# Performance work log

Hardware: AMD Instinct MI355X
Metric: run time of the kernel (lower is better)

## Reference

```python
import jax, jax.numpy as jnp
import numpy as np

N_EMBD = 256
HIDDEN = 20  # hardcoded in the module
B, L = 4096, 64


def setup_inputs() -> dict:
    key = jax.random.key(0)
    ks = jax.random.split(key, 12)
    s = 0.02
    return {
        "key": jax.random.normal(ks[0], (B, L, N_EMBD), dtype=jnp.float32),
        "value": jax.random.normal(ks[1], (B, L, N_EMBD), dtype=jnp.float32),
        "query": jax.random.normal(ks[2], (B, L, N_EMBD), dtype=jnp.float32),
        "Wk": jax.random.normal(ks[3], (N_EMBD, HIDDEN), dtype=jnp.float32) * s,
        "bk": jnp.zeros((HIDDEN,), dtype=jnp.float32),
        "Wq": jax.random.normal(ks[4], (N_EMBD, HIDDEN), dtype=jnp.float32) * s,
        "bq": jnp.zeros((HIDDEN,), dtype=jnp.float32),
        "Wv": jax.random.normal(ks[5], (N_EMBD, HIDDEN), dtype=jnp.float32) * s,
        "bv": jnp.zeros((HIDDEN,), dtype=jnp.float32),
        "Wp": jax.random.normal(ks[6], (HIDDEN, N_EMBD), dtype=jnp.float32) * s,
        "bp": jnp.zeros((N_EMBD,), dtype=jnp.float32),
    }


def reference(key, value, query, Wk, bk, Wq, bq, Wv, bv, Wp, bp):
    # projections: [B, L, D] -> [B, L, 20]
    ks = key @ Wk + bk
    qs = query @ Wq + bq
    vs = value @ Wv + bv

    # torch code normalizes by GLOBAL Frobenius norm iff both sums are nonzero
    cond = (jnp.sum(qs) != 0) & (jnp.sum(ks) != 0)
    qs = jnp.where(cond, qs / jnp.linalg.norm(qs), qs)
    ks = jnp.where(cond, ks / jnp.linalg.norm(ks), ks)

    N = qs.shape[0]  # B acts as the 'node' / reduction axis
    # kvs: reduce over dim0 ('l' in torch einsum) -> [L, m, d]
    kvs = jnp.einsum('nlm,nld->lmd', ks, vs)
    attention_num = jnp.einsum('nlm,lmd->nld', qs, kvs)  # [B, L, 20]
    attention_num = attention_num + jnp.sum(vs, axis=0)  # + vs_sum [L, 20]

    ks_sum = jnp.sum(ks, axis=0)  # [L, 20]
    attention_normalizer = jnp.einsum('nlm,lm->nl', qs, ks_sum)[..., None]  # [B, L, 1]
    attention_normalizer = attention_normalizer + jnp.asarray(N, dtype=qs.dtype)

    attn_output = attention_num / attention_normalizer  # [B, L, 20]
    return attn_output @ Wp + bp  # [B, L, D]
```

## Files before the change

kernel.cpp:

```cpp
#include <hip/hip_runtime.h>


namespace {
constexpr int D    = 256;
constexpr int H    = 20;
constexpr int LDIM = 64;
constexpr int BDIM = 4096;
constexpr int BL   = BDIM * LDIM;
constexpr int TPB  = 256;
constexpr int KC   = 64;
constexpr int TS   = 257;

constexpr int OFF_KVS  = 0;
constexpr int OFF_KSUM = OFF_KVS + LDIM * H * H;
constexpr int OFF_VSUM = OFF_KSUM + LDIM * H;
constexpr int OFF_SCAL = OFF_VSUM + LDIM * H;
constexpr int ACC_FLOATS = OFF_SCAL + 4;
constexpr int OFF_QS   = 28416;
}

__device__ __forceinline__ void project_one(
    const float* __restrict__ in, const float* __restrict__ W,
    const float* __restrict__ bias, float* __restrict__ out,
    float* tile, int base, int tid,
    float* sum_dst, float* ss_dst)
{
    float acc[H];
#pragma unroll
    for (int m = 0; m < H; ++m) acc[m] = 0.f;

    const float4* __restrict__ in4 = reinterpret_cast<const float4*>(in);

    for (int c = 0; c < 4; ++c) {
#pragma unroll
        for (int i = 0; i < 16; ++i) {
            int f = tid + i * TPB;
            int token = f >> 4;
            int kq    = f & 15;
            float4 v = in4[(size_t)(base + token) * (D / 4) + c * 16 + kq];
            int kk = kq * 4;
            tile[(kk + 0) * TS + token] = v.x;
            tile[(kk + 1) * TS + token] = v.y;
            tile[(kk + 2) * TS + token] = v.z;
            tile[(kk + 3) * TS + token] = v.w;
        }
        __syncthreads();

        const float* __restrict__ Wc = W + c * KC * H;
#pragma unroll 2
        for (int k = 0; k < KC; ++k) {
            float x = tile[k * TS + tid];
#pragma unroll
            for (int m = 0; m < H; ++m)
                acc[m] = fmaf(x, Wc[k * H + m], acc[m]);
        }
        __syncthreads();
    }

    float v[H];
    float s1 = 0.f, s2 = 0.f;
#pragma unroll
    for (int m = 0; m < H; ++m) {
        v[m] = acc[m] + bias[m];
        s1 += v[m];
        s2 = fmaf(v[m], v[m], s2);
    }
    float4* o4 = reinterpret_cast<float4*>(out + (size_t)(base + tid) * H);
    o4[0] = make_float4(v[0],  v[1],  v[2],  v[3]);
    o4[1] = make_float4(v[4],  v[5],  v[6],  v[7]);
    o4[2] = make_float4(v[8],  v[9],  v[10], v[11]);
    o4[3] = make_float4(v[12], v[13], v[14], v[15]);
    o4[4] = make_float4(v[16], v[17], v[18], v[19]);

    if (sum_dst) {
#pragma unroll
        for (int off = 32; off > 0; off >>= 1) {
            s1 += __shfl_down(s1, off);
            s2 += __shfl_down(s2, off);
        }
        if ((tid & 63) == 0) {
            atomicAdd(sum_dst, s1);
            atomicAdd(ss_dst, s2);
        }
    }
}

__global__ __launch_bounds__(TPB) void proj_kernel(
    const float* __restrict__ key, const float* __restrict__ value,
    const float* __restrict__ query,
    const float* __restrict__ Wk, const float* __restrict__ bk,
    const float* __restrict__ Wq, const float* __restrict__ bq,
    const float* __restrict__ Wv, const float* __restrict__ bv,
    float* __restrict__ qs, float* __restrict__ ks, float* __restrict__ vs,
    float* __restrict__ scalars)
{
    __shared__ float tile[KC * TS];
    const int tid  = threadIdx.x;
    const int base = blockIdx.x * TPB;

    project_one(key,   Wk, bk, ks, tile, base, tid, scalars + 1, scalars + 3);
    project_one(value, Wv, bv, vs, tile, base, tid, nullptr,     nullptr);
    project_one(query, Wq, bq, qs, tile, base, tid, scalars + 0, scalars + 2);
}

__global__ __launch_bounds__(TPB) void reduce_kernel(
    const float* __restrict__ ks, const float* __restrict__ vs,
    float* __restrict__ kvs, float* __restrict__ ks_sum, float* __restrict__ vs_sum)
{
    __shared__ float lks[64 * H];
    __shared__ float lvs[64 * H];
    const int tid   = threadIdx.x;
    const int l     = blockIdx.x & 63;
    const int split = blockIdx.x >> 6;
    const int n0    = split * 64;

    const float4* __restrict__ ks4 = reinterpret_cast<const float4*>(ks);
    const float4* __restrict__ vs4 = reinterpret_cast<const float4*>(vs);
    float4* lks4 = reinterpret_cast<float4*>(lks);
    float4* lvs4 = reinterpret_cast<float4*>(lvs);
    for (int id = tid; id < 64 * (H / 4); id += TPB) {
        int n = id / (H / 4), q = id % (H / 4);
        size_t g = ((size_t)(n0 + n) * LDIM + l) * (H / 4) + q;
        lks4[id] = ks4[g];
        lvs4[id] = vs4[g];
    }
    __syncthreads();

    const int s0 = tid, s1 = tid + 256;
    const int m0 = s0 / H, d0 = s0 % H;
    const int m1 = s1 / H, d1 = s1 % H;
    const bool has1 = (s1 < H * H);
    float a0 = 0.f, a1 = 0.f;
    for (int n = 0; n < 64; ++n) {
        const float* pk = lks + n * H;
        const float* pv = lvs + n * H;
        a0 = fmaf(pk[m0], pv[d0], a0);
        if (has1) a1 = fmaf(pk[m1], pv[d1], a1);
    }
    atomicAdd(&kvs[l * H * H + s0], a0);
    if (has1) atomicAdd(&kvs[l * H * H + s1], a1);

    if (tid < 2 * H) {
        const bool isk = tid < H;
        const int  m   = isk ? tid : tid - H;
        const float* src = isk ? lks : lvs;
        float s = 0.f;
        for (int n = 0; n < 64; ++n) s += src[n * H + m];
        atomicAdd(isk ? &ks_sum[l * H + m] : &vs_sum[l * H + m], s);
    }
}

__global__ __launch_bounds__(TPB) void out_kernel(
    const float* __restrict__ qs, const float* __restrict__ kvs,
    const float* __restrict__ ks_sum, const float* __restrict__ vs_sum,
    const float* __restrict__ scalars,
    const float* __restrict__ Wp, const float* __restrict__ bp,
    float* __restrict__ out)
{
    __shared__ float qsl[64 * H];
    __shared__ float attn[64 * H];
    __shared__ float nrm[64];
    const int tid = threadIdx.x;
    const size_t base = (size_t)blockIdx.x * 64;

    const float sum_q = scalars[0], sum_k = scalars[1];
    const float ss_q  = scalars[2], ss_k  = scalars[3];
    const bool  cond  = (sum_q != 0.f) && (sum_k != 0.f);
    const float scale = cond ? rsqrtf(ss_q) * rsqrtf(ss_k) : 1.f;

    const float4* __restrict__ qs4 = reinterpret_cast<const float4*>(qs) + base * (H / 4);
    float4* qsl4 = reinterpret_cast<float4*>(qsl);
    for (int id = tid; id < 64 * (H / 4); id += TPB) qsl4[id] = qs4[id];
    __syncthreads();

    if (tid < 64) {
        const int t = tid;
        float s = 0.f;
#pragma unroll
        for (int j = 0; j < H; ++j)
            s = fmaf(qsl[t * H + j], ks_sum[t * H + j], s);
        nrm[t] = fmaf(s, scale, (float)BDIM);
    }
    __syncthreads();

    for (int id = tid; id < 64 * H; id += TPB) {
        const int t = id / H, m = id % H;
        float s = 0.f;
#pragma unroll
        for (int j = 0; j < H; ++j)
            s = fmaf(qsl[t * H + j], kvs[t * H * H + j * H + m], s);
        attn[id] = (fmaf(s, scale, vs_sum[t * H + m])) / nrm[t];
    }
    __syncthreads();

    float wp[H];
#pragma unroll
    for (int m = 0; m < H; ++m) wp[m] = Wp[m * D + tid];
    const float bias = bp[tid];
    float* outp = out + base * D + tid;
    for (int t = 0; t < 64; ++t) {
        const float4* a4 = reinterpret_cast<const float4*>(attn + t * H);
        float acc = bias;
#pragma unroll
        for (int q = 0; q < H / 4; ++q) {
            float4 a = a4[q];
            acc = fmaf(a.x, wp[q * 4 + 0], acc);
            acc = fmaf(a.y, wp[q * 4 + 1], acc);
            acc = fmaf(a.z, wp[q * 4 + 2], acc);
            acc = fmaf(a.w, wp[q * 4 + 3], acc);
        }
        outp[(size_t)t * D] = acc;
    }
}

extern "C" void kernel_launch(void* const* d_in, const int* in_sizes, int n_in,
                              void* d_out, int out_size, void* d_ws, size_t ws_size,
                              hipStream_t stream)
{
    const float* key   = (const float*)d_in[0];
    const float* value = (const float*)d_in[1];
    const float* query = (const float*)d_in[2];
    const float* Wk    = (const float*)d_in[3];
    const float* bk    = (const float*)d_in[4];
    const float* Wq    = (const float*)d_in[5];
    const float* bq    = (const float*)d_in[6];
    const float* Wv    = (const float*)d_in[7];
    const float* bv    = (const float*)d_in[8];
    const float* Wp    = (const float*)d_in[9];
    const float* bp    = (const float*)d_in[10];

    float* ws      = (float*)d_ws;
    float* kvs     = ws + OFF_KVS;
    float* ks_sum  = ws + OFF_KSUM;
    float* vs_sum  = ws + OFF_VSUM;
    float* scalars = ws + OFF_SCAL;
    float* qs      = ws + OFF_QS;
    float* ks      = qs + (size_t)BL * H;
    float* vs      = ks + (size_t)BL * H;

    hipMemsetAsync(d_ws, 0, ACC_FLOATS * sizeof(float), stream);

    proj_kernel<<<BL / TPB, TPB, 0, stream>>>(key, value, query,
                                              Wk, bk, Wq, bq, Wv, bv,
                                              qs, ks, vs, scalars);
    reduce_kernel<<<LDIM * 64, TPB, 0, stream>>>(ks, vs, kvs, ks_sum, vs_sum);
    out_kernel<<<BDIM, TPB, 0, stream>>>(qs, kvs, ks_sum, vs_sum, scalars,
                                         Wp, bp, (float*)d_out);
}
```

Baseline: 1.126 ms.

## Split projection across grid.y, load rows directly, and halve reduce splits

The projection kernel now launches one block row per input tensor (key, value, query) via blockIdx.y. Each thread reads its own token's 256-float row straight from global memory with float4 loads, replacing the shared-memory transpose tile and its barriers. This is meant to cut LDS traffic and syncs and to raise occupancy. The cost is per-thread strided row reads that coalesce poorly. The reduce kernel uses 32 splits of 128 tokens instead of 64 splits of 64, halving the atomics, and the output loop gets an unroll hint.

```diff
diff --git a/kernel.cpp b/kernel.cpp
--- a/kernel.cpp
+++ b/kernel.cpp
@@ -8,8 +8,8 @@
 constexpr int BDIM = 4096;
 constexpr int BL   = BDIM * LDIM;
 constexpr int TPB  = 256;
-constexpr int KC   = 64;
-constexpr int TS   = 257;
+constexpr int NSPLIT = 32;
+constexpr int NCHUNK = BDIM / NSPLIT;
 
 constexpr int OFF_KVS  = 0;
 constexpr int OFF_KSUM = OFF_KVS + LDIM * H * H;
@@ -17,72 +17,6 @@
 constexpr int OFF_SCAL = OFF_VSUM + LDIM * H;
 constexpr int ACC_FLOATS = OFF_SCAL + 4;
 constexpr int OFF_QS   = 28416;
-}
-
-__device__ __forceinline__ void project_one(
-    const float* __restrict__ in, const float* __restrict__ W,
-    const float* __restrict__ bias, float* __restrict__ out,
-    float* tile, int base, int tid,
-    float* sum_dst, float* ss_dst)
-{
-    float acc[H];
-#pragma unroll
-    for (int m = 0; m < H; ++m) acc[m] = 0.f;
-
-    const float4* __restrict__ in4 = reinterpret_cast<const float4*>(in);
-
-    for (int c = 0; c < 4; ++c) {
-#pragma unroll
-        for (int i = 0; i < 16; ++i) {
-            int f = tid + i * TPB;
-            int token = f >> 4;
-            int kq    = f & 15;
-            float4 v = in4[(size_t)(base + token) * (D / 4) + c * 16 + kq];
-            int kk = kq * 4;
-            tile[(kk + 0) * TS + token] = v.x;
-            tile[(kk + 1) * TS + token] = v.y;
-            tile[(kk + 2) * TS + token] = v.z;
-            tile[(kk + 3) * TS + token] = v.w;
-        }
-        __syncthreads();
-
-        const float* __restrict__ Wc = W + c * KC * H;
-#pragma unroll 2
-        for (int k = 0; k < KC; ++k) {
-            float x = tile[k * TS + tid];
-#pragma unroll
-            for (int m = 0; m < H; ++m)
-                acc[m] = fmaf(x, Wc[k * H + m], acc[m]);
-        }
-        __syncthreads();
-    }
-
-    float v[H];
-    float s1 = 0.f, s2 = 0.f;
-#pragma unroll
-    for (int m = 0; m < H; ++m) {
-        v[m] = acc[m] + bias[m];
-        s1 += v[m];
-        s2 = fmaf(v[m], v[m], s2);
-    }
-    float4* o4 = reinterpret_cast<float4*>(out + (size_t)(base + tid) * H);
-    o4[0] = make_float4(v[0],  v[1],  v[2],  v[3]);
-    o4[1] = make_float4(v[4],  v[5],  v[6],  v[7]);
-    o4[2] = make_float4(v[8],  v[9],  v[10], v[11]);
-    o4[3] = make_float4(v[12], v[13], v[14], v[15]);
-    o4[4] = make_float4(v[16], v[17], v[18], v[19]);
-
-    if (sum_dst) {
-#pragma unroll
-        for (int off = 32; off > 0; off >>= 1) {
-            s1 += __shfl_down(s1, off);
-            s2 += __shfl_down(s2, off);
-        }
-        if ((tid & 63) == 0) {
-            atomicAdd(sum_dst, s1);
-            atomicAdd(ss_dst, s2);
-        }
-    }
 }
 
 __global__ __launch_bounds__(TPB) void proj_kernel(
@@ -94,31 +28,92 @@
     float* __restrict__ qs, float* __restrict__ ks, float* __restrict__ vs,
     float* __restrict__ scalars)
 {
-    __shared__ float tile[KC * TS];
-    const int tid  = threadIdx.x;
-    const int base = blockIdx.x * TPB;
-
-    project_one(key,   Wk, bk, ks, tile, base, tid, scalars + 1, scalars + 3);
-    project_one(value, Wv, bv, vs, tile, base, tid, nullptr,     nullptr);
-    project_one(query, Wq, bq, qs, tile, base, tid, scalars + 0, scalars + 2);
+    const int tid   = threadIdx.x;
+    const int which = blockIdx.y;
+
+    const float* in; const float* W; const float* bias; float* out;
+    float* sum_dst = nullptr; float* ss_dst = nullptr;
+    if (which == 0)      { in = key;   W = Wk; bias = bk; out = ks;
+                           sum_dst = scalars + 1; ss_dst = scalars + 3; }
+    else if (which == 1) { in = value; W = Wv; bias = bv; out = vs; }
+    else                 { in = query; W = Wq; bias = bq; out = qs;
+                           sum_dst = scalars + 0; ss_dst = scalars + 2; }
+
+    const size_t token = (size_t)blockIdx.x * TPB + tid;
+    const float4* __restrict__ row =
+        reinterpret_cast<const float4*>(in) + token * (D / 4);
+
+    float acc[H];
+#pragma unroll
+    for (int m = 0; m < H; ++m) acc[m] = 0.f;
+
+    for (int c = 0; c < 8; ++c) {
+        float4 x[8];
+#pragma unroll
+        for (int u = 0; u < 8; ++u) x[u] = row[c * 8 + u];
+
+        const float* __restrict__ Wc = W + c * 32 * H;
+#pragma unroll
+        for (int u = 0; u < 8; ++u) {
+            const float xv0 = x[u].x, xv1 = x[u].y, xv2 = x[u].z, xv3 = x[u].w;
+            const float* __restrict__ W0 = Wc + (u * 4 + 0) * H;
+            const float* __restrict__ W1 = Wc + (u * 4 + 1) * H;
+            const float* __restrict__ W2 = Wc + (u * 4 + 2) * H;
+            const float* __restrict__ W3 = Wc + (u * 4 + 3) * H;
+#pragma unroll
+            for (int m = 0; m < H; ++m) {
+                acc[m] = fmaf(xv0, W0[m], acc[m]);
+                acc[m] = fmaf(xv1, W1[m], acc[m]);
+                acc[m] = fmaf(xv2, W2[m], acc[m]);
+                acc[m] = fmaf(xv3, W3[m], acc[m]);
+            }
+        }
+    }
+
+    float v[H];
+    float s1 = 0.f, s2 = 0.f;
+#pragma unroll
+    for (int m = 0; m < H; ++m) {
+        v[m] = acc[m] + bias[m];
+        s1 += v[m];
+        s2 = fmaf(v[m], v[m], s2);
+    }
+    float4* o4 = reinterpret_cast<float4*>(out + token * H);
+    o4[0] = make_float4(v[0],  v[1],  v[2],  v[3]);
+    o4[1] = make_float4(v[4],  v[5],  v[6],  v[7]);
+    o4[2] = make_float4(v[8],  v[9],  v[10], v[11]);
+    o4[3] = make_float4(v[12], v[13], v[14], v[15]);
+    o4[4] = make_float4(v[16], v[17], v[18], v[19]);
+
+    if (sum_dst) {
+#pragma unroll
+        for (int off = 32; off > 0; off >>= 1) {
+            s1 += __shfl_down(s1, off);
+            s2 += __shfl_down(s2, off);
+        }
+        if ((tid & 63) == 0) {
+            atomicAdd(sum_dst, s1);
+            atomicAdd(ss_dst, s2);
+        }
+    }
 }
 
 __global__ __launch_bounds__(TPB) void reduce_kernel(
     const float* __restrict__ ks, const float* __restrict__ vs,
     float* __restrict__ kvs, float* __restrict__ ks_sum, float* __restrict__ vs_sum)
 {
-    __shared__ float lks[64 * H];
-    __shared__ float lvs[64 * H];
+    __shared__ float lks[NCHUNK * H];
+    __shared__ float lvs[NCHUNK * H];
     const int tid   = threadIdx.x;
     const int l     = blockIdx.x & 63;
     const int split = blockIdx.x >> 6;
-    const int n0    = split * 64;
+    const int n0    = split * NCHUNK;
 
     const float4* __restrict__ ks4 = reinterpret_cast<const float4*>(ks);
     const float4* __restrict__ vs4 = reinterpret_cast<const float4*>(vs);
     float4* lks4 = reinterpret_cast<float4*>(lks);
     float4* lvs4 = reinterpret_cast<float4*>(lvs);
-    for (int id = tid; id < 64 * (H / 4); id += TPB) {
+    for (int id = tid; id < NCHUNK * (H / 4); id += TPB) {
         int n = id / (H / 4), q = id % (H / 4);
         size_t g = ((size_t)(n0 + n) * LDIM + l) * (H / 4) + q;
         lks4[id] = ks4[g];
@@ -131,7 +126,7 @@
     const int m1 = s1 / H, d1 = s1 % H;
     const bool has1 = (s1 < H * H);
     float a0 = 0.f, a1 = 0.f;
-    for (int n = 0; n < 64; ++n) {
+    for (int n = 0; n < NCHUNK; ++n) {
         const float* pk = lks + n * H;
         const float* pv = lvs + n * H;
         a0 = fmaf(pk[m0], pv[d0], a0);
@@ -145,7 +140,7 @@
         const int  m   = isk ? tid : tid - H;
         const float* src = isk ? lks : lvs;
         float s = 0.f;
-        for (int n = 0; n < 64; ++n) s += src[n * H + m];
+        for (int n = 0; n < NCHUNK; ++n) s += src[n * H + m];
         atomicAdd(isk ? &ks_sum[l * H + m] : &vs_sum[l * H + m], s);
     }
 }
@@ -198,6 +193,7 @@
     for (int m = 0; m < H; ++m) wp[m] = Wp[m * D + tid];
     const float bias = bp[tid];
     float* outp = out + base * D + tid;
+#pragma unroll 4
     for (int t = 0; t < 64; ++t) {
         const float4* a4 = reinterpret_cast<const float4*>(attn + t * H);
         float acc = bias;
@@ -240,10 +236,10 @@
 
     hipMemsetAsync(d_ws, 0, ACC_FLOATS * sizeof(float), stream);
 
-    proj_kernel<<<BL / TPB, TPB, 0, stream>>>(key, value, query,
-                                              Wk, bk, Wq, bq, Wv, bv,
-                                              qs, ks, vs, scalars);
-    reduce_kernel<<<LDIM * 64, TPB, 0, stream>>>(ks, vs, kvs, ks_sum, vs_sum);
+    proj_kernel<<<dim3(BL / TPB, 3), TPB, 0, stream>>>(key, value, query,
+                                                       Wk, bk, Wq, bq, Wv, bv,
+                                                       qs, ks, vs, scalars);
+    reduce_kernel<<<LDIM * NSPLIT, TPB, 0, stream>>>(ks, vs, kvs, ks_sum, vs_sum);
     out_kernel<<<BDIM, TPB, 0, stream>>>(qs, kvs, ks_sum, vs_sum, scalars,
                                          Wp, bp, (float*)d_out);
 }
```

After: 996.5 us. 1.13x faster.
